# Kernel tuning notes

Hardware: AMD Instinct MI355X
Metric: run time of the kernel (lower is better)

## Reference

```python
import jax, jax.numpy as jnp
import numpy as np

D_FEATURE = 1024
HEAD = 16
D_K = 64
D_V = 64
EPS = 1e-6


def setup_inputs() -> dict:
    key = jax.random.key(0)
    ks = jax.random.split(key, 12)
    B, S = 2, 2048
    s_in = 1.0 / np.sqrt(D_FEATURE)
    s_o = 1.0 / np.sqrt(HEAD * D_V)
    return {
        "q": jax.random.normal(ks[0], (B, S, D_FEATURE), jnp.float32),
        "k": jax.random.normal(ks[1], (B, S, D_FEATURE), jnp.float32),
        "v": jax.random.normal(ks[2], (B, S, D_FEATURE), jnp.float32),
        "Wq": jax.random.uniform(ks[3], (D_FEATURE, HEAD * D_K), jnp.float32, -s_in, s_in),
        "bq": jnp.zeros((HEAD * D_K,), jnp.float32),
        "Wk": jax.random.uniform(ks[4], (D_FEATURE, HEAD * D_K), jnp.float32, -s_in, s_in),
        "bk": jnp.zeros((HEAD * D_K,), jnp.float32),
        "Wv": jax.random.uniform(ks[5], (D_FEATURE, HEAD * D_V), jnp.float32, -s_in, s_in),
        "bv": jnp.zeros((HEAD * D_V,), jnp.float32),
        "Wo": jax.random.uniform(ks[6], (HEAD * D_V, D_FEATURE), jnp.float32, -s_o, s_o),
        "bo": jnp.zeros((D_FEATURE,), jnp.float32),
        "gamma": jnp.ones((D_FEATURE,), jnp.float32),
        "beta": jnp.zeros((D_FEATURE,), jnp.float32),
    }


def reference(q, k, v, Wq, bq, Wk, bk, Wv, bv, Wo, bo, gamma, beta):
    B, Sq, _ = q.shape
    Sk, Sv = k.shape[1], v.shape[1]
    shortcut = v
    # projections -> (b, h, s, d)
    qh = (q @ Wq + bq).reshape(B, Sq, HEAD, D_K).transpose(0, 2, 1, 3)
    kh = (k @ Wk + bk).reshape(B, Sk, HEAD, D_K).transpose(0, 2, 1, 3)
    vh = (v @ Wv + bv).reshape(B, Sv, HEAD, D_V).transpose(0, 2, 1, 3)
    scale = 1.0 / np.sqrt(D_K).astype(np.float32)
    scores = jnp.einsum('bhqd,bhkd->bhqk', qh * scale, kh)
    attn = jax.nn.softmax(scores, axis=-1)  # dropout is identity (p=0 / eval)
    ctx = jnp.einsum('bhqk,bhkd->bhqd', attn, vh)
    ctx = ctx.transpose(0, 2, 1, 3).reshape(B, Sv, HEAD * D_V)
    out = ctx @ Wo + bo
    out = out + shortcut
    # LayerNorm, eps=1e-6
    mu = out.mean(-1, keepdims=True)
    var = out.var(-1, keepdims=True)
    out = (out - mu) * jax.lax.rsqrt(var + EPS) * gamma + beta
    return out
```

## Files before the change

kernel.cpp:

```cpp
#include <hip/hip_runtime.h>

#define D_FEAT 1024
#define NTOK   4096
#define SEQ    2048
#define NHEAD  16
#define DK     64
#define QSCALE 0.1803368801111204f

typedef float          f32x4  __attribute__((ext_vector_type(4)));
typedef float          f32x16 __attribute__((ext_vector_type(16)));
typedef short          s16x8  __attribute__((ext_vector_type(8)));
typedef unsigned short u16x4  __attribute__((ext_vector_type(4)));

__device__ __forceinline__ unsigned short f2bf(float f) {
  union { float f; unsigned int u; } x; x.f = f;
  unsigned int r = x.u + 0x7fffu + ((x.u >> 16) & 1u);
  return (unsigned short)(r >> 16);
}
__device__ __forceinline__ unsigned short f2h(float f) {
  union { _Float16 h; unsigned short u; } x; x.h = (_Float16)f; return x.u;
}
__device__ __forceinline__ float h2f(unsigned short u) {
  union { _Float16 h; unsigned short u; } x; x.u = u; return (float)x.h;
}

__device__ __forceinline__ f32x4 mfma16(s16x8 a, s16x8 b, f32x4 c) {
  return __builtin_amdgcn_mfma_f32_16x16x32_bf16(a, b, c, 0, 0, 0);
}
__device__ __forceinline__ f32x16 mfma32(s16x8 a, s16x8 b, f32x16 c) {
  return __builtin_amdgcn_mfma_f32_32x32x16_bf16(a, b, c, 0, 0, 0);
}

__device__ __forceinline__ void gload16(const void* g, void* l) {
  __builtin_amdgcn_global_load_lds(
      (const __attribute__((address_space(1))) void*)g,
      (__attribute__((address_space(3))) void*)l, 16, 0, 0);
}

__device__ __forceinline__ float fexp2(float x) {
  return __builtin_amdgcn_exp2f(x);
}

__device__ __forceinline__ unsigned int cvtpk(float a, float b) {
  unsigned int r;
  asm("v_cvt_pk_bf16_f32 %0, %1, %2" : "=v"(r) : "v"(a), "v"(b));
  return r;
}
__device__ __forceinline__ void swap32(unsigned int& x, unsigned int& y) {
  asm("v_permlane32_swap_b32 %0, %1" : "+v"(x), "+v"(y));
}
__device__ __forceinline__ s16x8 mk8(unsigned int a, unsigned int b,
                                     unsigned int c, unsigned int d) {
  union { unsigned int u[4]; s16x8 v; } x;
  x.u[0] = a; x.u[1] = b; x.u[2] = c; x.u[3] = d; return x.v;
}

__global__ __launch_bounds__(256) void prep_kernel(
    const float* __restrict__ q, const float* __restrict__ k, const float* __restrict__ v,
    const float* __restrict__ Wq, const float* __restrict__ Wk,
    const float* __restrict__ Wv, const float* __restrict__ Wo,
    unsigned short* __restrict__ qb, unsigned short* __restrict__ kb,
    unsigned short* __restrict__ vb,
    unsigned short* __restrict__ WT, unsigned short* __restrict__ Wot)
{
  __shared__ float tile[32][33];
  const int bx = blockIdx.x, tid = threadIdx.x;
  if (bx < 12288) {
    int sel = bx >> 12;
    const float* src = sel == 0 ? q : (sel == 1 ? k : v);
    unsigned short* dst = sel == 0 ? qb : (sel == 1 ? kb : vb);
    size_t i = ((size_t)(bx & 4095) * 256 + tid) * 4;
    float4 f = *(const float4*)(src + i);
    u16x4 o; o.x = f2bf(f.x); o.y = f2bf(f.y); o.z = f2bf(f.z); o.w = f2bf(f.w);
    *(u16x4*)(dst + i) = o;
  } else {
    int t = bx - 12288;
    int z = t >> 10, rest = t & 1023;
    int bxt = rest & 31, byt = rest >> 5;
    const float* W = z == 0 ? Wq : z == 1 ? Wk : z == 2 ? Wv : Wo;
    unsigned short* T = (z < 3) ? (WT + (size_t)z * 1024 * 1024) : Wot;
    int tx = tid & 31, ty = tid >> 5;
    int n = bxt * 32 + tx;
    for (int i = 0; i < 4; ++i) {
      int kk = byt * 32 + ty + i * 8;
      tile[ty + i * 8][tx] = W[(size_t)kk * D_FEAT + n];
    }
    __syncthreads();
    int kk = byt * 32 + tx;
    for (int i = 0; i < 4; ++i) {
      int n2 = bxt * 32 + ty + i * 8;
      T[(size_t)n2 * D_FEAT + kk] = f2bf(tile[tx][ty + i * 8]);
    }
  }
}

__global__ __launch_bounds__(256, 2) void gemm_qkv(
    const unsigned short* __restrict__ qb, const unsigned short* __restrict__ kb,
    const unsigned short* __restrict__ vb, const unsigned short* __restrict__ WT,
    const float* __restrict__ bq, const float* __restrict__ bk, const float* __restrict__ bv,
    unsigned short* __restrict__ Qp, unsigned short* __restrict__ Kp, unsigned short* __restrict__ Vt)
{
  __shared__ __align__(16) unsigned short sAB[2][2 * 128 * 64];
  const int tid = threadIdx.x;
  const int wave = tid >> 6, lane = tid & 63;
  const int quad = lane >> 4, l16 = lane & 15;
  const int wx = wave & 1, wy = wave >> 1;
  const int bx = blockIdx.x;
  const int chunk = bx >> 3;

  const unsigned short* rA;
  const unsigned short* rB;
  int m0, n0;
  if (chunk < 2) {
    m0 = blockIdx.y * 128; n0 = (bx & 7) * 128;
    rA = (chunk ? kb : qb) + (size_t)m0 * D_FEAT;
    rB = WT + (size_t)(chunk * 1024 + n0) * D_FEAT;
  } else {
    m0 = (bx & 7) * 128; n0 = blockIdx.y * 128;
    rA = WT + (size_t)(2048 + m0) * D_FEAT;
    rB = vb + (size_t)n0 * D_FEAT;
  }

  f32x4 acc[4][4];
  for (int mt = 0; mt < 4; ++mt)
    for (int nt = 0; nt < 4; ++nt) acc[mt][nt] = (f32x4){0.f, 0.f, 0.f, 0.f};

  const int rw8 = lane >> 3;
  const int cls = ((lane & 7) ^ (lane >> 3)) * 8;
  const int sw = l16 & 7;

#define QKV_ISSUE(BUF, K0)                                                     \
  _Pragma("unroll") for (int j = 0; j < 4; ++j) {                              \
    int ch = wave * 4 + j;                                                     \
    gload16(rA + (size_t)(ch * 8 + rw8) * D_FEAT + (K0) + cls,                 \
            &sAB[BUF][ch * 512]);                                              \
    gload16(rB + (size_t)(ch * 8 + rw8) * D_FEAT + (K0) + cls,                 \
            &sAB[BUF][128 * 64 + ch * 512]);                                   \
  }

#define QKV_COMP(BUF)                                                         \
  {                                                                            \
    const unsigned short* sA = &sAB[BUF][0];                                   \
    const unsigned short* sB = &sAB[BUF][128 * 64];                            \
    s16x8 af[2][4], bfr[2][4];                                                 \
    _Pragma("unroll") for (int kk = 0; kk < 2; ++kk) {                         \
      int c = ((kk * 4 + quad) ^ sw) * 8;                                      \
      _Pragma("unroll") for (int mt = 0; mt < 4; ++mt)                         \
        af[kk][mt] = *(const s16x8*)(sA + (wy * 64 + mt * 16 + l16) * 64 + c); \
      _Pragma("unroll") for (int nt = 0; nt < 4; ++nt)                         \
        bfr[kk][nt] = *(const s16x8*)(sB + (wx * 64 + nt * 16 + l16) * 64 + c);\
    }                                                                          \
    _Pragma("unroll") for (int kk = 0; kk < 2; ++kk)                           \
      _Pragma("unroll") for (int mt = 0; mt < 4; ++mt)                         \
        _Pragma("unroll") for (int nt = 0; nt < 4; ++nt)                       \
          acc[mt][nt] = mfma16(af[kk][mt], bfr[kk][nt], acc[mt][nt]);          \
  }

#define GSYNC(N)                                                               \
  asm volatile("s_waitcnt vmcnt(" #N ")" ::: "memory");                        \
  __builtin_amdgcn_s_barrier();                                               \
  __builtin_amdgcn_sched_barrier(0);

  QKV_ISSUE(0, 0);
  QKV_ISSUE(1, 64);
  for (int t2 = 0; t2 < 14; t2 += 2) {
    GSYNC(8);
    QKV_COMP(0);
    __builtin_amdgcn_s_barrier();
    __builtin_amdgcn_sched_barrier(0);
    QKV_ISSUE(0, (t2 + 2) * 64);
    GSYNC(8);
    QKV_COMP(1);
    __builtin_amdgcn_s_barrier();
    __builtin_amdgcn_sched_barrier(0);
    QKV_ISSUE(1, (t2 + 3) * 64);
  }
  GSYNC(8);
  QKV_COMP(0);
  GSYNC(0);
  QKV_COMP(1);
#undef QKV_ISSUE
#undef QKV_COMP
#undef GSYNC

  if (chunk < 2) {
    const float* bias = chunk ? bk : bq;
    unsigned short* Cp = chunk ? Kp : Qp;
    const float scale = chunk == 0 ? QSCALE : 1.0f;
    for (int mt = 0; mt < 4; ++mt)
      for (int nt = 0; nt < 4; ++nt) {
        int col = n0 + wx * 64 + nt * 16 + l16;
        float bcol = bias[col];
        for (int r = 0; r < 4; ++r) {
          int row = m0 + wy * 64 + mt * 16 + quad * 4 + r;
          Cp[(size_t)row * D_FEAT + col] = f2bf((acc[mt][nt][r] + bcol) * scale);
        }
      }
  } else {
    for (int mt = 0; mt < 4; ++mt)
      for (int r = 0; r < 4; ++r) {
        float bfeat = bv[m0 + wy * 64 + mt * 16 + quad * 4 + r];
        for (int nt = 0; nt < 4; ++nt) acc[mt][nt][r] += bfeat;
      }
    unsigned short* tb = &sAB[0][0];
    for (int p = 0; p < 2; ++p) {
      __syncthreads();
      if (wx == p) {
        for (int mt = 0; mt < 4; ++mt)
          for (int nt = 0; nt < 4; ++nt) {
            int tok_loc = nt * 16 + l16;
            for (int r = 0; r < 4; ++r) {
              int f_loc = wy * 64 + mt * 16 + quad * 4 + r;
              tb[f_loc * 72 + tok_loc] = f2bf(acc[mt][nt][r]);
            }
          }
      }
      __syncthreads();
      int n_base = n0 + p * 64;
      int b = n_base >> 11, tok0 = n_base & 2047;
      int ck = lane & 7;
      for (int j = 0; j < 4; ++j) {
        int f_loc = (wave * 4 + j) * 8 + rw8;
        int f = m0 + f_loc, hh = f >> 6, dv = f & 63;
        *(s16x8*)(Vt + ((size_t)(b * 16 + hh) * 64 + dv) * SEQ + tok0 + ck * 8) =
            *(const s16x8*)(tb + f_loc * 72 + ck * 8);
      }
    }
  }
}

__global__ __launch_bounds__(256) void gemm_o(
    const unsigned short* __restrict__ A, const unsigned short* __restrict__ Bt,
    const float* __restrict__ bias, const float* __restrict__ resid,
    float* __restrict__ Cout)
{
  __shared__ __align__(16) unsigned short sA2[2][128 * 64];
  __shared__ __align__(16) unsigned short sB2[2][64 * 64];
  const int tid = threadIdx.x;
  const int wave = tid >> 6, lane = tid & 63;
  const int quad = lane >> 4, l16 = lane & 15;
  const int wx = wave & 1, wy = wave >> 1;
  const int n0 = blockIdx.x * 64, m0 = blockIdx.y * 128;

  f32x4 acc[4][2];
  for (int mt = 0; mt < 4; ++mt)
    for (int nt = 0; nt < 2; ++nt) acc[mt][nt] = (f32x4){0.f, 0.f, 0.f, 0.f};

  const int rw8 = lane >> 3;
  const int cls = ((lane & 7) ^ (lane >> 3)) * 8;
  const int sw = l16 & 7;

#define O_ISSUE(BUF, K0)                                                       \
  _Pragma("unroll") for (int j = 0; j < 4; ++j) {                              \
    int ch = wave * 4 + j;                                                     \
    gload16(A + (size_t)(m0 + ch * 8 + rw8) * D_FEAT + (K0) + cls,             \
            &sA2[BUF][ch * 512]);                                              \
  }                                                                            \
  _Pragma("unroll") for (int j = 0; j < 2; ++j) {                              \
    int ch = wave * 2 + j;                                                     \
    gload16(Bt + (size_t)(n0 + ch * 8 + rw8) * D_FEAT + (K0) + cls,            \
            &sB2[BUF][ch * 512]);                                              \
  }

#define O_COMP(BUF)                                                           \
  {                                                                            \
    const unsigned short* sA = &sA2[BUF][0];                                   \
    const unsigned short* sB = &sB2[BUF][0];                                   \
    s16x8 af[2][4], bfr[2][2];                                                 \
    _Pragma("unroll") for (int kk = 0; kk < 2; ++kk) {                         \
      int c = ((kk * 4 + quad) ^ sw) * 8;                                      \
      _Pragma("unroll") for (int mt = 0; mt < 4; ++mt)                         \
        af[kk][mt] = *(const s16x8*)(sA + (wy * 64 + mt * 16 + l16) * 64 + c); \
      _Pragma("unroll") for (int nt = 0; nt < 2; ++nt)                         \
        bfr[kk][nt] = *(const s16x8*)(sB + (wx * 32 + nt * 16 + l16) * 64 + c);\
    }                                                                          \
    _Pragma("unroll") for (int kk = 0; kk < 2; ++kk)                           \
      _Pragma("unroll") for (int mt = 0; mt < 4; ++mt)                         \
        _Pragma("unroll") for (int nt = 0; nt < 2; ++nt)                       \
          acc[mt][nt] = mfma16(af[kk][mt], bfr[kk][nt], acc[mt][nt]);          \
  }

#define GSYNC(N)                                                               \
  asm volatile("s_waitcnt vmcnt(" #N ")" ::: "memory");                        \
  __builtin_amdgcn_s_barrier();                                               \
  __builtin_amdgcn_sched_barrier(0);

  O_ISSUE(0, 0);
  O_ISSUE(1, 64);
  for (int t2 = 0; t2 < 14; t2 += 2) {
    GSYNC(6);
    O_COMP(0);
    __builtin_amdgcn_s_barrier();
    __builtin_amdgcn_sched_barrier(0);
    O_ISSUE(0, (t2 + 2) * 64);
    GSYNC(6);
    O_COMP(1);
    __builtin_amdgcn_s_barrier();
    __builtin_amdgcn_sched_barrier(0);
    O_ISSUE(1, (t2 + 3) * 64);
  }
  GSYNC(6);
  O_COMP(0);
  GSYNC(0);
  O_COMP(1);
#undef O_ISSUE
#undef O_COMP
#undef GSYNC

  for (int mt = 0; mt < 4; ++mt)
    for (int nt = 0; nt < 2; ++nt) {
      int col = n0 + wx * 32 + nt * 16 + l16;
      float bcol = bias[col];
      for (int r = 0; r < 4; ++r) {
        int row = m0 + wy * 64 + mt * 16 + quad * 4 + r;
        Cout[(size_t)row * D_FEAT + col] =
            acc[mt][nt][r] + bcol + resid[(size_t)row * D_FEAT + col];
      }
    }
}

__global__ __launch_bounds__(256, 3) void flash_part(
    const unsigned short* __restrict__ Qp,
    const unsigned short* __restrict__ Kp,
    const unsigned short* __restrict__ Vt,
    unsigned short* __restrict__ Opart,
    float* __restrict__ L)
{
  __shared__ __align__(16) unsigned short sB4[4][4096];

  const int tid = threadIdx.x;
  const int wave = tid >> 6, lane = tid & 63;
  const int l32 = lane & 31, h = lane >> 5;

  const int blk = blockIdx.x;
  const int xcd = blk & 7, jj = blk >> 3;
  const int grp = xcd * 8 + (jj >> 4);
  const int q0 = (jj & 15) * 128;
  const int bh = grp & 31, z = grp >> 5;
  const int b = bh >> 4, hd = bh & 15;
  const int kbase = z * (SEQ / 2);
  const size_t base = (size_t)b * SEQ * D_FEAT + (size_t)hd * DK;
  const unsigned short* vt = Vt + (size_t)bh * 64 * SEQ;

  const int qrow = wave * 32 + l32;

  const unsigned short* qptr = Qp + base + (size_t)(q0 + qrow) * D_FEAT;
  s16x8 bq[4];
#pragma unroll
  for (int s = 0; s < 4; ++s)
    bq[s] = *(const s16x8*)(qptr + (2 * s + h) * 8);

  const int krow = tid >> 3;
  const unsigned short* kPtr =
      Kp + base + (size_t)(kbase + krow) * D_FEAT + (((tid & 7) ^ (krow & 7)) * 8);
  const int vrow = tid >> 2;
  const unsigned short* vPtr =
      vt + (size_t)vrow * SEQ + kbase + (((tid & 3) ^ ((tid >> 3) & 3)) * 8);

  const int kdst = wave * 512;
#pragma unroll
  for (int pb = 0; pb < 2; ++pb) {
    gload16(kPtr, &sB4[pb][kdst]);
    gload16(vPtr, &sB4[pb][2048 + kdst]);
    kPtr += 32 * D_FEAT; vPtr += 32;
  }

  f32x16 o0, o1, stE, stO;
#pragma unroll
  for (int r = 0; r < 16; ++r) { o0[r] = 0.f; o1[r] = 0.f; }
  float lsA = 0.f, lsB = 0.f;

  const int kxor = l32 & 7;
  const int vxor = (l32 >> 1) & 3;

#define QK_TILE(BUF, ST)                                                       \
  {                                                                            \
    const unsigned short* bK = &sB4[BUF][0];                                   \
    _Pragma("unroll") for (int r = 0; r < 16; ++r) ST[r] = 0.f;                \
    __builtin_amdgcn_s_setprio(1);                                            \
    _Pragma("unroll") for (int s = 0; s < 4; ++s) {                            \
      s16x8 a = *(const s16x8*)(bK + l32 * 64 + (((2 * s + h) ^ kxor) * 8));   \
      ST = mfma32(a, bq[s], ST);                                               \
    }                                                                          \
    __builtin_amdgcn_s_setprio(0);                                            \
  }

#define SMPV_TILE(BUFV, ST)                                                    \
  {                                                                            \
    const unsigned short* bV = &sB4[BUFV][2048];                               \
    unsigned int c[8];                                                         \
    _Pragma("unroll") for (int i = 0; i < 8; ++i) {                            \
      float e0 = fexp2(ST[2 * i]);                                             \
      float e1 = fexp2(ST[2 * i + 1]);                                         \
      lsA += e0; lsB += e1;                                                    \
      c[i] = cvtpk(e0, e1);                                                    \
    }                                                                          \
    swap32(c[0], c[2]); swap32(c[1], c[3]);                                    \
    swap32(c[4], c[6]); swap32(c[5], c[7]);                                    \
    s16x8 bp0 = mk8(c[0], c[1], c[2], c[3]);                                   \
    s16x8 bp1 = mk8(c[4], c[5], c[6], c[7]);                                   \
    __builtin_amdgcn_s_setprio(1);                                            \
    _Pragma("unroll") for (int kk = 0; kk < 2; ++kk) {                         \
      int cs = ((2 * kk + h) ^ vxor) * 8;                                      \
      s16x8 av0 = *(const s16x8*)(bV + l32 * 32 + cs);                         \
      s16x8 av1 = *(const s16x8*)(bV + (32 + l32) * 32 + cs);                  \
      s16x8 bp = kk ? bp1 : bp0;                                               \
      o0 = mfma32(av0, bp, o0);                                                \
      o1 = mfma32(av1, bp, o1);                                                \
    }                                                                          \
    __builtin_amdgcn_s_setprio(0);                                            \
  }

#define SYNC2                                                                  \
  asm volatile("s_waitcnt vmcnt(2)" ::: "memory");                             \
  __builtin_amdgcn_s_barrier();                                               \
  __builtin_amdgcn_sched_barrier(0);
#define ISSUE(NXT)                                                             \
  gload16(kPtr, &sB4[NXT][kdst]);                                              \
  gload16(vPtr, &sB4[NXT][2048 + kdst]);                                       \
  kPtr += 32 * D_FEAT; vPtr += 32;

  SYNC2; ISSUE(2); QK_TILE(0, stE);
  SYNC2; ISSUE(3); QK_TILE(1, stO); SMPV_TILE(0, stE);
  SYNC2; ISSUE(0); QK_TILE(2, stE); SMPV_TILE(1, stO);
  SYNC2; ISSUE(1); QK_TILE(3, stO); SMPV_TILE(2, stE);
  for (int g6 = 0; g6 < 6; ++g6) {
    SYNC2; ISSUE(2); QK_TILE(0, stE); SMPV_TILE(3, stO);
    SYNC2; ISSUE(3); QK_TILE(1, stO); SMPV_TILE(0, stE);
    SYNC2; ISSUE(0); QK_TILE(2, stE); SMPV_TILE(1, stO);
    SYNC2; ISSUE(1); QK_TILE(3, stO); SMPV_TILE(2, stE);
  }
  SYNC2; ISSUE(2); QK_TILE(0, stE); SMPV_TILE(3, stO);
  SYNC2; ISSUE(3); QK_TILE(1, stO); SMPV_TILE(0, stE);
  SYNC2;           QK_TILE(2, stE); SMPV_TILE(1, stO);
  asm volatile("s_waitcnt vmcnt(0)" ::: "memory");
  __builtin_amdgcn_s_barrier();
  __builtin_amdgcn_sched_barrier(0);
  QK_TILE(3, stO); SMPV_TILE(2, stE);
  SMPV_TILE(3, stO);
#undef QK_TILE
#undef SMPV_TILE
#undef SYNC2
#undef ISSUE

  float lsum = lsA + lsB;
  lsum += __shfl_xor(lsum, 32, 64);
  const size_t trow = (size_t)(z * 32 + bh) * SEQ + (q0 + qrow);
  unsigned short* orow = Opart + trow * 64;
#pragma unroll
  for (int g = 0; g < 4; ++g) {
    u16x4 ov;
    for (int r = 0; r < 4; ++r) ov[r] = f2h(o0[4 * g + r]);
    *(u16x4*)(orow + 8 * g + 4 * h) = ov;
  }
#pragma unroll
  for (int g = 0; g < 4; ++g) {
    u16x4 ov;
    for (int r = 0; r < 4; ++r) ov[r] = f2h(o1[4 * g + r]);
    *(u16x4*)(orow + 32 + 8 * g + 4 * h) = ov;
  }
  if (h == 0) L[trow] = lsum;
}

__global__ __launch_bounds__(256) void combine_kernel(
    const unsigned short* __restrict__ Opart, const float* __restrict__ L,
    unsigned short* __restrict__ ctx)
{
  const int idx = blockIdx.x * 256 + threadIdx.x;
  const int dq = idx & 15;
  const int trow = idx >> 4;
  const int bh = trow >> 11, tok = trow & 2047;
  const int b = bh >> 4, h = bh & 15;
  const int HS = 32 * SEQ;

  float inv = __builtin_amdgcn_rcpf(L[trow] + L[HS + trow]);

  u16x4 p0 = *(const u16x4*)(Opart + (size_t)trow * 64 + dq * 4);
  u16x4 p1 = *(const u16x4*)(Opart + ((size_t)HS + trow) * 64 + dq * 4);
  u16x4 o;
  for (int r = 0; r < 4; ++r)
    o[r] = f2bf((h2f(p0[r]) + h2f(p1[r])) * inv);
  *(u16x4*)(ctx + (size_t)b * SEQ * D_FEAT + (size_t)tok * D_FEAT + h * 64 + dq * 4) = o;
}

__global__ __launch_bounds__(256) void ln_kernel(
    const float* __restrict__ x, const float* __restrict__ gamma,
    const float* __restrict__ beta, float* __restrict__ out)
{
  const int row = blockIdx.x, tid = threadIdx.x;
  const int wave = tid >> 6, lane = tid & 63;
  const float* xr = x + (size_t)row * D_FEAT;
  float4 v = ((const float4*)xr)[tid];
  float s  = v.x + v.y + v.z + v.w;
  float ss = v.x * v.x + v.y * v.y + v.z * v.z + v.w * v.w;
  for (int off = 1; off < 64; off <<= 1) {
    s  += __shfl_xor(s,  off, 64);
    ss += __shfl_xor(ss, off, 64);
  }
  __shared__ float red[8];
  if (lane == 0) { red[wave] = s; red[wave + 4] = ss; }
  __syncthreads();
  s  = red[0] + red[1] + red[2] + red[3];
  ss = red[4] + red[5] + red[6] + red[7];
  float mean = s * (1.f / D_FEAT);
  float var  = ss * (1.f / D_FEAT) - mean * mean;
  float rstd = rsqrtf(var + 1e-6f);
  float4 g  = ((const float4*)gamma)[tid];
  float4 bt = ((const float4*)beta)[tid];
  float4 o;
  o.x = (v.x - mean) * rstd * g.x + bt.x;
  o.y = (v.y - mean) * rstd * g.y + bt.y;
  o.z = (v.z - mean) * rstd * g.z + bt.z;
  o.w = (v.w - mean) * rstd * g.w + bt.w;
  ((float4*)(out + (size_t)row * D_FEAT))[tid] = o;
}

extern "C" void kernel_launch(void* const* d_in, const int* in_sizes, int n_in,
                              void* d_out, int out_size, void* d_ws, size_t ws_size,
                              hipStream_t stream) {
  const float* q     = (const float*)d_in[0];
  const float* k     = (const float*)d_in[1];
  const float* v     = (const float*)d_in[2];
  const float* Wq    = (const float*)d_in[3];
  const float* bq    = (const float*)d_in[4];
  const float* Wk    = (const float*)d_in[5];
  const float* bk    = (const float*)d_in[6];
  const float* Wv    = (const float*)d_in[7];
  const float* bv    = (const float*)d_in[8];
  const float* Wo    = (const float*)d_in[9];
  const float* bo    = (const float*)d_in[10];
  const float* gamma = (const float*)d_in[11];
  const float* beta  = (const float*)d_in[12];

  char* w = (char*)d_ws;
  const size_t MB = 1u << 20;
  unsigned short* qb    = (unsigned short*)(w + 0 * MB);
  unsigned short* kb    = (unsigned short*)(w + 8 * MB);
  unsigned short* vb    = (unsigned short*)(w + 16 * MB);
  unsigned short* WT    = (unsigned short*)(w + 24 * MB);
  unsigned short* Wot   = (unsigned short*)(w + 30 * MB);
  unsigned short* Qp    = (unsigned short*)(w + 32 * MB);
  unsigned short* Kp    = (unsigned short*)(w + 40 * MB);
  unsigned short* Vt    = (unsigned short*)(w + 48 * MB);
  unsigned short* ctx   = (unsigned short*)(w + 56 * MB);
  float*          tmp   = (float*)(w + 64 * MB);
  unsigned short* Opart = (unsigned short*)(w + 0 * MB);
  float*          L     = (float*)(w + 16 * MB);

  prep_kernel<<<16384, 256, 0, stream>>>(q, k, v, Wq, Wk, Wv, Wo, qb, kb, vb, WT, Wot);

  gemm_qkv<<<dim3(24, 32), 256, 0, stream>>>(qb, kb, vb, WT, bq, bk, bv, Qp, Kp, Vt);

  flash_part<<<1024, 256, 0, stream>>>(Qp, Kp, Vt, Opart, L);

  combine_kernel<<<4096, 256, 0, stream>>>(Opart, L, ctx);

  gemm_o<<<dim3(16, 32), 256, 0, stream>>>(ctx, Wot, bo, v, tmp);

  ln_kernel<<<NTOK, 256, 0, stream>>>(tmp, gamma, beta, (float*)d_out);
}
```

Measured before the change: 227.8 us.

## Fuse split-KV combine into output projection GEMM A-tile loading

Removes the separate combine kernel and has gemm_o read both fp16 flash partials directly. It sums them, scales by the reciprocal of the summed row-sums (precomputed into LDS per block) and converts to bf16 while staging A tiles through registers into LDS. The B operand moves to a triple-buffered async pipeline. This saves one launch and the ctx write/read round trip, but each gemm_o block now reads twice the A bytes and does the conversion redundantly across the 16 column blocks, using more registers and LDS.

```diff
diff --git a/kernel.cpp b/kernel.cpp
--- a/kernel.cpp
+++ b/kernel.cpp
@@ -230,17 +230,21 @@
 }
 
 __global__ __launch_bounds__(256) void gemm_o(
-    const unsigned short* __restrict__ A, const unsigned short* __restrict__ Bt,
+    const unsigned short* __restrict__ Opart, const float* __restrict__ L,
+    const unsigned short* __restrict__ Bt,
     const float* __restrict__ bias, const float* __restrict__ resid,
     float* __restrict__ Cout)
 {
   __shared__ __align__(16) unsigned short sA2[2][128 * 64];
-  __shared__ __align__(16) unsigned short sB2[2][64 * 64];
+  __shared__ __align__(16) unsigned short sB3[3][64 * 64];
+  __shared__ float invLds[16 * 128];
   const int tid = threadIdx.x;
   const int wave = tid >> 6, lane = tid & 63;
   const int quad = lane >> 4, l16 = lane & 15;
   const int wx = wave & 1, wy = wave >> 1;
   const int n0 = blockIdx.x * 64, m0 = blockIdx.y * 128;
+  const int b16 = (m0 >> 11) * 16;
+  const int tokbase = m0 & 2047;
 
   f32x4 acc[4][2];
   for (int mt = 0; mt < 4; ++mt)
@@ -250,22 +254,52 @@
   const int cls = ((lane & 7) ^ (lane >> 3)) * 8;
   const int sw = l16 & 7;
 
-#define O_ISSUE(BUF, K0)                                                       \
+  {
+    int hh = tid >> 4, tl = (tid & 15) * 8;
+    size_t l0 = (size_t)(b16 + hh) * 2048 + tokbase + tl;
+#pragma unroll
+    for (int e = 0; e < 8; ++e)
+      invLds[hh * 128 + tl + e] =
+          __builtin_amdgcn_rcpf(L[l0 + e] + L[l0 + e + 65536]);
+  }
+
+  uint4 pE0[4], pE1[4], pO0[4], pO1[4];
+
+#define A_LOAD(P0, P1, T)                                                      \
   _Pragma("unroll") for (int j = 0; j < 4; ++j) {                              \
     int ch = wave * 4 + j;                                                     \
-    gload16(A + (size_t)(m0 + ch * 8 + rw8) * D_FEAT + (K0) + cls,             \
-            &sA2[BUF][ch * 512]);                                              \
-  }                                                                            \
+    size_t trow = (size_t)(b16 + (T)) * 2048 + tokbase + ch * 8 + rw8;         \
+    P0[j] = *(const uint4*)(Opart + trow * 64 + cls);                          \
+    P1[j] = *(const uint4*)(Opart + (trow + 65536) * 64 + cls);                \
+  }
+
+#define CVTW(U0, U1, W)                                                        \
+  { float lo_ = (h2f((unsigned short)(U0)) + h2f((unsigned short)(U1))) * inv; \
+    float hi_ = (h2f((unsigned short)((U0) >> 16)) +                           \
+                 h2f((unsigned short)((U1) >> 16))) * inv;                     \
+    W = cvtpk(lo_, hi_); }
+
+#define A_WRITE(P0, P1, T, BUFA)                                               \
+  _Pragma("unroll") for (int j = 0; j < 4; ++j) {                              \
+    float inv = invLds[(T) * 128 + wave * 32 + j * 8 + rw8];                   \
+    unsigned int w0, w1, w2, w3;                                               \
+    CVTW(P0[j].x, P1[j].x, w0); CVTW(P0[j].y, P1[j].y, w1);                    \
+    CVTW(P0[j].z, P1[j].z, w2); CVTW(P0[j].w, P1[j].w, w3);                    \
+    *(s16x8*)(&sA2[BUFA][(wave * 4 + j) * 512 + lane * 8]) =                   \
+        mk8(w0, w1, w2, w3);                                                   \
+  }
+
+#define B_ISSUE(T, BUF)                                                        \
   _Pragma("unroll") for (int j = 0; j < 2; ++j) {                              \
     int ch = wave * 2 + j;                                                     \
-    gload16(Bt + (size_t)(n0 + ch * 8 + rw8) * D_FEAT + (K0) + cls,            \
-            &sB2[BUF][ch * 512]);                                              \
-  }
-
-#define O_COMP(BUF)                                                           \
+    gload16(Bt + (size_t)(n0 + ch * 8 + rw8) * D_FEAT + (T) * 64 + cls,        \
+            &sB3[BUF][ch * 512]);                                              \
+  }
+
+#define O_COMP(BA, BB)                                                         \
   {                                                                            \
-    const unsigned short* sA = &sA2[BUF][0];                                   \
-    const unsigned short* sB = &sB2[BUF][0];                                   \
+    const unsigned short* sA = &sA2[BA][0];                                    \
+    const unsigned short* sB = &sB3[BB][0];                                    \
     s16x8 af[2][4], bfr[2][2];                                                 \
     _Pragma("unroll") for (int kk = 0; kk < 2; ++kk) {                         \
       int c = ((kk * 4 + quad) ^ sw) * 8;                                      \
@@ -280,32 +314,43 @@
           acc[mt][nt] = mfma16(af[kk][mt], bfr[kk][nt], acc[mt][nt]);          \
   }
 
-#define GSYNC(N)                                                               \
-  asm volatile("s_waitcnt vmcnt(" #N ")" ::: "memory");                        \
+#define TOPSYNC(N)                                                             \
+  asm volatile("s_waitcnt vmcnt(" #N ") lgkmcnt(0)" ::: "memory");             \
   __builtin_amdgcn_s_barrier();                                               \
   __builtin_amdgcn_sched_barrier(0);
 
-  O_ISSUE(0, 0);
-  O_ISSUE(1, 64);
-  for (int t2 = 0; t2 < 14; t2 += 2) {
-    GSYNC(6);
-    O_COMP(0);
-    __builtin_amdgcn_s_barrier();
-    __builtin_amdgcn_sched_barrier(0);
-    O_ISSUE(0, (t2 + 2) * 64);
-    GSYNC(6);
-    O_COMP(1);
-    __builtin_amdgcn_s_barrier();
-    __builtin_amdgcn_sched_barrier(0);
-    O_ISSUE(1, (t2 + 3) * 64);
-  }
-  GSYNC(6);
-  O_COMP(0);
-  GSYNC(0);
-  O_COMP(1);
-#undef O_ISSUE
+  A_LOAD(pE0, pE1, 0); B_ISSUE(0, 0);
+  A_LOAD(pO0, pO1, 1); B_ISSUE(1, 1);
+  __syncthreads();
+  A_WRITE(pE0, pE1, 0, 0);
+  A_WRITE(pO0, pO1, 1, 1);
+  A_LOAD(pE0, pE1, 2); B_ISSUE(2, 2);
+  asm volatile("s_waitcnt lgkmcnt(0)" ::: "memory");
+  __builtin_amdgcn_s_barrier();
+  __builtin_amdgcn_sched_barrier(0);
+  O_COMP(0, 0);
+
+  TOPSYNC(2); A_WRITE(pE0, pE1,  2, 0); A_LOAD(pO0, pO1,  3); B_ISSUE( 3, 0); O_COMP(1, 1);
+  TOPSYNC(2); A_WRITE(pO0, pO1,  3, 1); A_LOAD(pE0, pE1,  4); B_ISSUE( 4, 1); O_COMP(0, 2);
+  TOPSYNC(2); A_WRITE(pE0, pE1,  4, 0); A_LOAD(pO0, pO1,  5); B_ISSUE( 5, 2); O_COMP(1, 0);
+  TOPSYNC(2); A_WRITE(pO0, pO1,  5, 1); A_LOAD(pE0, pE1,  6); B_ISSUE( 6, 0); O_COMP(0, 1);
+  TOPSYNC(2); A_WRITE(pE0, pE1,  6, 0); A_LOAD(pO0, pO1,  7); B_ISSUE( 7, 1); O_COMP(1, 2);
+  TOPSYNC(2); A_WRITE(pO0, pO1,  7, 1); A_LOAD(pE0, pE1,  8); B_ISSUE( 8, 2); O_COMP(0, 0);
+  TOPSYNC(2); A_WRITE(pE0, pE1,  8, 0); A_LOAD(pO0, pO1,  9); B_ISSUE( 9, 0); O_COMP(1, 1);
+  TOPSYNC(2); A_WRITE(pO0, pO1,  9, 1); A_LOAD(pE0, pE1, 10); B_ISSUE(10, 1); O_COMP(0, 2);
+  TOPSYNC(2); A_WRITE(pE0, pE1, 10, 0); A_LOAD(pO0, pO1, 11); B_ISSUE(11, 2); O_COMP(1, 0);
+  TOPSYNC(2); A_WRITE(pO0, pO1, 11, 1); A_LOAD(pE0, pE1, 12); B_ISSUE(12, 0); O_COMP(0, 1);
+  TOPSYNC(2); A_WRITE(pE0, pE1, 12, 0); A_LOAD(pO0, pO1, 13); B_ISSUE(13, 1); O_COMP(1, 2);
+  TOPSYNC(2); A_WRITE(pO0, pO1, 13, 1); A_LOAD(pE0, pE1, 14); B_ISSUE(14, 2); O_COMP(0, 0);
+  TOPSYNC(2); A_WRITE(pE0, pE1, 14, 0); A_LOAD(pO0, pO1, 15); B_ISSUE(15, 0); O_COMP(1, 1);
+  TOPSYNC(2); A_WRITE(pO0, pO1, 15, 1);                                       O_COMP(0, 2);
+  TOPSYNC(0);                                                                 O_COMP(1, 0);
+#undef A_LOAD
+#undef CVTW
+#undef A_WRITE
+#undef B_ISSUE
 #undef O_COMP
-#undef GSYNC
+#undef TOPSYNC
 
   for (int mt = 0; mt < 4; ++mt)
     for (int nt = 0; nt < 2; ++nt) {
@@ -462,27 +507,6 @@
   if (h == 0) L[trow] = lsum;
 }
 
-__global__ __launch_bounds__(256) void combine_kernel(
-    const unsigned short* __restrict__ Opart, const float* __restrict__ L,
-    unsigned short* __restrict__ ctx)
-{
-  const int idx = blockIdx.x * 256 + threadIdx.x;
-  const int dq = idx & 15;
-  const int trow = idx >> 4;
-  const int bh = trow >> 11, tok = trow & 2047;
-  const int b = bh >> 4, h = bh & 15;
-  const int HS = 32 * SEQ;
-
-  float inv = __builtin_amdgcn_rcpf(L[trow] + L[HS + trow]);
-
-  u16x4 p0 = *(const u16x4*)(Opart + (size_t)trow * 64 + dq * 4);
-  u16x4 p1 = *(const u16x4*)(Opart + ((size_t)HS + trow) * 64 + dq * 4);
-  u16x4 o;
-  for (int r = 0; r < 4; ++r)
-    o[r] = f2bf((h2f(p0[r]) + h2f(p1[r])) * inv);
-  *(u16x4*)(ctx + (size_t)b * SEQ * D_FEAT + (size_t)tok * D_FEAT + h * 64 + dq * 4) = o;
-}
-
 __global__ __launch_bounds__(256) void ln_kernel(
     const float* __restrict__ x, const float* __restrict__ gamma,
     const float* __restrict__ beta, float* __restrict__ out)
@@ -542,7 +566,6 @@
   unsigned short* Qp    = (unsigned short*)(w + 32 * MB);
   unsigned short* Kp    = (unsigned short*)(w + 40 * MB);
   unsigned short* Vt    = (unsigned short*)(w + 48 * MB);
-  unsigned short* ctx   = (unsigned short*)(w + 56 * MB);
   float*          tmp   = (float*)(w + 64 * MB);
   unsigned short* Opart = (unsigned short*)(w + 0 * MB);
   float*          L     = (float*)(w + 16 * MB);
@@ -553,9 +576,7 @@
 
   flash_part<<<1024, 256, 0, stream>>>(Qp, Kp, Vt, Opart, L);
 
-  combine_kernel<<<4096, 256, 0, stream>>>(Opart, L, ctx);
-
-  gemm_o<<<dim3(16, 32), 256, 0, stream>>>(ctx, Wot, bo, v, tmp);
+  gemm_o<<<dim3(16, 32), 256, 0, stream>>>(Opart, L, Wot, bo, v, tmp);
 
   ln_kernel<<<NTOK, 256, 0, stream>>>(tmp, gamma, beta, (float*)d_out);
 }
```

Measured after the change: 240.0 us. 5.4% more time.
